# Kernel tuning notes

Hardware: AMD Instinct MI355X
Metric: run time of the kernel (lower is better)

The kernel has to match this reference:

```python
import jax, jax.numpy as jnp
import numpy as np

N_TOKENS = 2048
HIDDEN = 2880
N_HEADS = 64          # total query heads
N_KV = 8              # key/value heads
Q_MULT = N_HEADS // N_KV
HEAD_DIM = 64
SLIDING_WINDOW = 128  # layer_idx=0 -> sliding-window layer
SM_SCALE = 1.0 / np.sqrt(HEAD_DIM)
RMS_EPS = 1e-5
ROPE_BASE = 150000.0
ROPE_SCALING = 32.0
INIT_CTX = 4096
NTK_ALPHA = 1.0
NTK_BETA = 32.0


def _rope_tables(num_tokens):
    # YaRN NTK-by-parts inverse frequencies (static constants)
    freq = ROPE_BASE ** (np.arange(0, HEAD_DIM, 2, dtype=np.float64) / HEAD_DIM)
    concentration = 0.1 * np.log(ROPE_SCALING) + 1.0
    d_half = HEAD_DIM / 2
    low = d_half * np.log(INIT_CTX / (NTK_BETA * 2 * np.pi)) / np.log(ROPE_BASE)
    high = d_half * np.log(INIT_CTX / (NTK_ALPHA * 2 * np.pi)) / np.log(ROPE_BASE)
    interpolation = 1.0 / (ROPE_SCALING * freq)
    extrapolation = 1.0 / freq
    ramp = (np.arange(d_half) - low) / (high - low)
    m = 1.0 - np.clip(ramp, 0.0, 1.0)
    inv_freq = interpolation * (1.0 - m) + extrapolation * m
    t = np.arange(num_tokens, dtype=np.float64)
    freqs = np.outer(t, inv_freq)
    cos = jnp.asarray((np.cos(freqs) * concentration), dtype=jnp.float32)
    sin = jnp.asarray((np.sin(freqs) * concentration), dtype=jnp.float32)
    return cos, sin  # [num_tokens, HEAD_DIM//2]


def _apply_rotary(x, cos, sin):
    # x: [n, heads, HEAD_DIM]
    c = cos[:, None, :].astype(x.dtype)
    s = sin[:, None, :].astype(x.dtype)
    x1, x2 = jnp.split(x, 2, axis=-1)
    return jnp.concatenate([x1 * c - x2 * s, x2 * c + x1 * s], axis=-1)


def setup_inputs() -> dict:
    key = jax.random.key(0)
    ks = jax.random.split(key, 7)
    return {
        "x": jax.random.normal(ks[0], (N_TOKENS, HIDDEN), jnp.float32),
        "scale": jax.random.uniform(ks[1], (HIDDEN,), jnp.float32, 0.5, 1.5),
        "sink": jax.random.normal(ks[2], (N_HEADS,), jnp.float32),
        "w_qkv": jax.random.normal(ks[3], (HIDDEN, (N_HEADS + 2 * N_KV) * HEAD_DIM), jnp.float32) * 0.02,
        "b_qkv": jax.random.normal(ks[4], ((N_HEADS + 2 * N_KV) * HEAD_DIM,), jnp.float32) * 0.02,
        "w_o": jax.random.normal(ks[5], (N_HEADS * HEAD_DIM, HIDDEN), jnp.float32) * 0.02,
        "b_o": jax.random.normal(ks[6], (HIDDEN,), jnp.float32) * 0.02,
    }


def reference(x, scale, sink, w_qkv, b_qkv, w_o, b_o):
    n = x.shape[0]
    # RMSNorm (fp32)
    t = x.astype(jnp.float32)
    rms = jnp.sqrt(jnp.mean(t * t, axis=-1, keepdims=True) + RMS_EPS)
    t = (t / rms) * scale

    # QKV projection + split
    qkv = t @ w_qkv + b_qkv
    q_sz = N_HEADS * HEAD_DIM
    kv_sz = N_KV * HEAD_DIM
    q = qkv[:, :q_sz].reshape(n, N_HEADS, HEAD_DIM)
    k = qkv[:, q_sz:q_sz + kv_sz].reshape(n, N_KV, HEAD_DIM)
    v = qkv[:, q_sz + kv_sz:].reshape(n, N_KV, HEAD_DIM)

    # RoPE (YaRN)
    cos, sin = _rope_tables(n)
    q = _apply_rotary(q, cos, sin)
    k = _apply_rotary(k, cos, sin)

    # GQA layout: [n, N_KV, Q_MULT, HEAD_DIM]
    qg = q.reshape(n, N_KV, Q_MULT, HEAD_DIM)

    # scores: [N_KV, Q_MULT, n_q, n_kv]
    scores = jnp.einsum('nhgd,mhd->hgnm', qg, k) * SM_SCALE

    # causal + sliding-window mask
    q_pos = jnp.arange(n)[:, None]
    kv_pos = jnp.arange(n)[None, :]
    mask = jnp.where(kv_pos > q_pos, -jnp.inf, 0.0)
    mask = mask + jnp.where((SLIDING_WINDOW > 0) & (q_pos - kv_pos > SLIDING_WINDOW), -jnp.inf, 0.0)
    scores = scores + mask[None, None, :, :].astype(scores.dtype)

    # sink logit appended as extra softmax column, then dropped
    s_col = jnp.broadcast_to(sink.reshape(N_KV, Q_MULT, 1, 1), (N_KV, Q_MULT, n, 1))
    w = jax.nn.softmax(jnp.concatenate([scores, s_col], axis=-1), axis=-1)[..., :-1]

    attn = jnp.einsum('hgnm,mhd->nhgd', w, v).reshape(n, N_HEADS * HEAD_DIM)
    out = attn @ w_o + b_o
    return x + out


if __name__ == '__main__':
    inp = setup_inputs()
    y = reference(**inp)
    print(y.shape, y.dtype)
```

## Files before the change

### kernel.cpp

```cpp
#include <hip/hip_runtime.h>
#include <cstdint>
#include <cstddef>

#define HIDDEN   2880
#define QKV_N    5120
#define OPROJ_K  4096
#define NTOK     2048
#define WIN      128
#define SM_SCALE 0.125f

typedef _Float16 half8  __attribute__((ext_vector_type(8)));
typedef _Float16 half4v __attribute__((ext_vector_type(4)));
typedef float    f32x4  __attribute__((ext_vector_type(4)));

__device__ __forceinline__ void gload16(const void* g, void* l) {
  __builtin_amdgcn_global_load_lds((__attribute__((address_space(1))) void*)g,
                                   (__attribute__((address_space(3))) void*)l,
                                   16, 0, 0);
}

__device__ __forceinline__ _Float16 f2h(float f) { return (_Float16)f; }

#define NB_T0  (80 * 45)
#define NB_T1  (46 * 64)
#define NB_ROPE 256

__device__ __forceinline__ void cast_transpose64(const float* __restrict__ W,
                                                 _Float16* __restrict__ Wt,
                                                 int K, int N, int n0, int k0,
                                                 float* tile ) {
  int t = threadIdx.x;
  #pragma unroll
  for (int p = 0; p < 16; ++p) {
    int r = p * 4 + (t >> 6), cc = t & 63;
    float vv = 0.f;
    if (n0 + cc < N) vv = W[(size_t)(k0 + r) * N + n0 + cc];
    tile[r * 65 + cc] = vv;
  }
  __syncthreads();
  #pragma unroll
  for (int p = 0; p < 2; ++p) {
    int idx = p * 256 + t;
    int r = idx >> 3, ch = (idx & 7) * 8;
    half8 h;
    #pragma unroll
    for (int u = 0; u < 8; ++u) h[u] = (_Float16)tile[(ch + u) * 65 + r];
    *(half8*)&Wt[(size_t)(n0 + r) * K + k0 + ch] = h;
  }
}

__global__ __launch_bounds__(256) void prep_kernel(const float* __restrict__ x,
                                                   const float* __restrict__ scale,
                                                   const float* __restrict__ w_qkv,
                                                   const float* __restrict__ w_o,
                                                   _Float16* __restrict__ a_h,
                                                   _Float16* __restrict__ wtq,
                                                   _Float16* __restrict__ wto,
                                                   float2* __restrict__ tab) {
  __shared__ float smem[64 * 65];
  int b = blockIdx.x, t = threadIdx.x;
  if (b < NB_T0) {
    cast_transpose64(w_qkv, wtq, HIDDEN, QKV_N, (b % 80) * 64, (b / 80) * 64, smem);
    return;
  }
  b -= NB_T0;
  if (b < NB_T1) {
    cast_transpose64(w_o, wto, OPROJ_K, HIDDEN, (b % 46) * 64, (b / 46) * 64, smem);
    return;
  }
  b -= NB_T1;
  if (b < NTOK) {
    int row = b;
    const float4* xr = (const float4*)(x + (size_t)row * HIDDEN);
    const float4* sc = (const float4*)scale;
    float4 v0 = xr[t];
    float4 v1 = xr[t + 256];
    float4 v2 = (t < 208) ? xr[t + 512] : make_float4(0.f, 0.f, 0.f, 0.f);
    float ss = v0.x*v0.x + v0.y*v0.y + v0.z*v0.z + v0.w*v0.w
             + v1.x*v1.x + v1.y*v1.y + v1.z*v1.z + v1.w*v1.w
             + v2.x*v2.x + v2.y*v2.y + v2.z*v2.z + v2.w*v2.w;
    #pragma unroll
    for (int m = 1; m < 64; m <<= 1) ss += __shfl_xor(ss, m, 64);
    if ((t & 63) == 0) smem[t >> 6] = ss;
    __syncthreads();
    float inv = 1.0f / sqrtf((smem[0] + smem[1] + smem[2] + smem[3]) * (1.0f / HIDDEN) + 1e-5f);
    _Float16* orow = a_h + (size_t)row * HIDDEN;
    auto store4 = [&](int c4, const float4& v, const float4& s) {
      half4v h;
      h[0] = f2h(v.x * inv * s.x); h[1] = f2h(v.y * inv * s.y);
      h[2] = f2h(v.z * inv * s.z); h[3] = f2h(v.w * inv * s.w);
      *(half4v*)(orow + (size_t)c4 * 4) = h;
    };
    store4(t, v0, sc[t]);
    store4(t + 256, v1, sc[t + 256]);
    if (t < 208) store4(t + 512, v2, sc[t + 512]);
    return;
  }
  b -= NTOK;
  {
    int idx = b * 256 + t;
    int tok = idx >> 5, d = idx & 31;
    const double PI = 3.14159265358979323846;
    double i = (double)d;
    double lf = log(150000.0);
    double freq = exp(lf * (i / 32.0));
    double interp = 1.0 / (32.0 * freq);
    double extrap = 1.0 / freq;
    double low  = 32.0 * log(4096.0 / (32.0 * 2.0 * PI)) / lf;
    double high = 32.0 * log(4096.0 / (2.0 * PI)) / lf;
    double ramp = (i - low) / (high - low);
    double mm = 1.0 - fmin(fmax(ramp, 0.0), 1.0);
    double invf = interp * (1.0 - mm) + extrap * mm;
    double ang = (double)tok * invf;
    double conc = 0.1 * log(32.0) + 1.0;
    tab[idx] = make_float2((float)(cos(ang) * conc), (float)(sin(ang) * conc));
  }
}

template <int BM, bool QKV_MODE, int MINW, bool SWZ>
__global__ __launch_bounds__(256, MINW) void gemm_kernel(const _Float16* __restrict__ A,
                                                         const _Float16* __restrict__ Bt,
                                                         const float* __restrict__ bias,
                                                         const float* __restrict__ resid,
                                                         const float2* __restrict__ tab,
                                                         void* __restrict__ Cout,
                                                         int M, int N, int K) {
  constexpr int MI = BM / 32;
  constexpr int NA = BM / 32;
  __shared__ _Float16 Alds[BM * 64];
  __shared__ _Float16 Blds[128 * 64];
  int tid = threadIdx.x;
  int wave = tid >> 6, lane = tid & 63;
  int wm = wave >> 1, wn = wave & 1;
  int c = lane & 15, quad = lane >> 4;
  int bx = blockIdx.x, by = blockIdx.y;
  if (SWZ) {
    int gx = gridDim.x;
    int flat = by * gx + bx;
    int n8 = (gx * gridDim.y) >> 3;
    int swz = (flat & 7) * n8 + (flat >> 3);
    bx = swz % gx; by = swz / gx;
  }
  int m0 = by * BM, n0 = bx * 128;

  const _Float16* gAp[NA]; _Float16* lAp[NA];
  #pragma unroll
  for (int i = 0; i < NA; ++i) {
    int p = wave * 64 + i * 256 + lane;
    int r = p >> 3;
    int kl = (p & 7) ^ (r & 7);
    gAp[i] = A + (size_t)(m0 + r) * K + kl * 8;
    lAp[i] = Alds + (size_t)(wave * 64 + i * 256) * 8;
  }
  const _Float16* gBp[4]; _Float16* lBp[4];
  #pragma unroll
  for (int i = 0; i < 4; ++i) {
    int p = wave * 64 + i * 256 + lane;
    int r = p >> 3;
    int kl = (p & 7) ^ (r & 7);
    gBp[i] = Bt + (size_t)(n0 + r) * K + kl * 8;
    lBp[i] = Blds + (size_t)(wave * 64 + i * 256) * 8;
  }

  int px[2];
  px[0] = ((0 * 4 + quad) ^ (c & 7)) * 8;
  px[1] = ((1 * 4 + quad) ^ (c & 7)) * 8;

  f32x4 acc[MI][4] = {};
  int nIter = K >> 6;
  for (int kt = 0; kt < nIter; ++kt) {
    __syncthreads();
    #pragma unroll
    for (int i = 0; i < NA; ++i) { gload16(gAp[i], lAp[i]); gAp[i] += 64; }
    #pragma unroll
    for (int i = 0; i < 4; ++i)  { gload16(gBp[i], lBp[i]); gBp[i] += 64; }
    __syncthreads();
    half8 a[MI][2], b[4][2];
    #pragma unroll
    for (int i = 0; i < MI; ++i) {
      int row = wm * (BM / 2) + i * 16 + c;
      a[i][0] = *(const half8*)&Alds[row * 64 + px[0]];
      a[i][1] = *(const half8*)&Alds[row * 64 + px[1]];
    }
    #pragma unroll
    for (int j = 0; j < 4; ++j) {
      int row = wn * 64 + j * 16 + c;
      b[j][0] = *(const half8*)&Blds[row * 64 + px[0]];
      b[j][1] = *(const half8*)&Blds[row * 64 + px[1]];
    }
    #pragma unroll
    for (int i = 0; i < MI; ++i)
      #pragma unroll
      for (int j = 0; j < 4; ++j) {
        acc[i][j] = __builtin_amdgcn_mfma_f32_16x16x32_f16(a[i][0], b[j][0], acc[i][j], 0, 0, 0);
        acc[i][j] = __builtin_amdgcn_mfma_f32_16x16x32_f16(a[i][1], b[j][1], acc[i][j], 0, 0, 0);
      }
  }

  if (QKV_MODE) {
    _Float16* outp = (_Float16*)Cout;
    bool ropeTile = (n0 < 4608);
    #pragma unroll
    for (int i = 0; i < MI; ++i) {
      int rowb = m0 + wm * (BM / 2) + i * 16 + quad * 4;
      if (ropeTile) {
        #pragma unroll
        for (int jp = 0; jp < 2; ++jp) {
          int col = n0 + wn * 64 + jp * 16 + c;
          float b1 = bias[col], b2 = bias[col + 32];
          #pragma unroll
          for (int r = 0; r < 4; ++r) {
            float2 cs = tab[(size_t)(rowb + r) * 32 + jp * 16 + c];
            float x1 = acc[i][jp][r] + b1;
            float x2 = acc[i][jp + 2][r] + b2;
            outp[(size_t)(rowb + r) * QKV_N + col]      = f2h(x1 * cs.x - x2 * cs.y);
            outp[(size_t)(rowb + r) * QKV_N + col + 32] = f2h(x2 * cs.x + x1 * cs.y);
          }
        }
      } else {
        #pragma unroll
        for (int j = 0; j < 4; ++j) {
          int col = n0 + wn * 64 + j * 16 + c;
          float bv = bias[col];
          #pragma unroll
          for (int r = 0; r < 4; ++r)
            outp[(size_t)(rowb + r) * QKV_N + col] = f2h(acc[i][j][r] + bv);
        }
      }
    }
  } else {
    float* outp = (float*)Cout;
    #pragma unroll
    for (int i = 0; i < MI; ++i) {
      int rowb = m0 + wm * (BM / 2) + i * 16 + quad * 4;
      #pragma unroll
      for (int j = 0; j < 4; ++j) {
        int col = n0 + wn * 64 + j * 16 + c;
        if (col < N) {
          float bv = bias[col];
          #pragma unroll
          for (int r = 0; r < 4; ++r)
            outp[(size_t)(rowb + r) * N + col] =
                acc[i][j][r] + bv + resid[(size_t)(rowb + r) * N + col];
        }
      }
    }
  }
}

#define TQ 16
__global__ __launch_bounds__(256) void attn_kernel(const _Float16* __restrict__ qkv,
                                                   const float* __restrict__ sink,
                                                   _Float16* __restrict__ attn_out) {
  __shared__ __align__(16) char smem[61440];
  _Float16* Klds = (_Float16*)smem;
  _Float16* Qlds = (_Float16*)(smem + 20480);
  _Float16* Ps   = (_Float16*)smem;
  _Float16* Vt   = (_Float16*)(smem + 40960);

  int qt = blockIdx.x, kvh = blockIdx.y;
  int Q0 = qt * TQ;
  int kmin = (Q0 >= WIN) ? Q0 - WIN : 0;
  int nkv = Q0 + TQ - kmin;
  int tid = threadIdx.x;
  int wave = tid >> 6, lane = tid & 63;
  int c = lane & 15, quad = lane >> 4;

  {
    const _Float16* kbase = qkv + 4096 + kvh * 64;
    #pragma unroll
    for (int p = 0; p < 5; ++p) {
      int ci = p * 256 + wave * 64 + lane;
      int row = ci >> 3, pc = ci & 7;
      int lc = pc ^ (row & 7);
      gload16(kbase + (size_t)(kmin + row) * QKV_N + lc * 8,
              (char*)Klds + (size_t)(p * 256 + wave * 64) * 16);
    }
  }
  {
    const _Float16* qbase = qkv + kvh * 512;
    #pragma unroll
    for (int p = 0; p < 4; ++p) {
      int ci = p * 256 + wave * 64 + lane;
      int tok = ci >> 6, Lp = ci & 63;
      int Llog = (Lp & 56) | ((Lp ^ tok) & 7);
      gload16(qbase + (size_t)(Q0 + tok) * QKV_N + Llog * 8,
              (char*)Qlds + (size_t)(p * 256 + wave * 64) * 16);
    }
  }
  #pragma unroll
  for (int p = 0; p < 5; ++p) {
    int cc = p * 256 + tid;
    int col = cc % 160;
    int d0 = (cc / 160) * 8;
    union { uint4 u4; _Float16 hv[8]; } buf;
    if (col < nkv) buf.u4 = *(const uint4*)(qkv + (size_t)(kmin + col) * QKV_N + 4608 + kvh * 64 + d0);
    else           buf.u4 = make_uint4(0, 0, 0, 0);
    #pragma unroll
    for (int uu = 0; uu < 8; ++uu) Vt[(d0 + uu) * 160 + col] = buf.hv[uu];
  }

  __syncthreads();

  half8 aq[2][2];
  #pragma unroll
  for (int i = 0; i < 2; ++i) {
    int qm = wave * 2 + i;
    #pragma unroll
    for (int ks = 0; ks < 2; ++ks) {
      int kc = ks * 4 + quad;
      int Lp = qm * 8 + (kc ^ (c & 7));
      aq[i][ks] = *(const half8*)&Qlds[c * 512 + Lp * 8];
    }
  }

  f32x4 sacc[2][9] = {};
  #pragma unroll
  for (int j = 0; j < 9; ++j) {
    #pragma unroll
    for (int ks = 0; ks < 2; ++ks) {
      int kc = ks * 4 + quad;
      int pc = kc ^ (c & 7);
      half8 bk = *(const half8*)&Klds[(j * 16 + c) * 64 + pc * 8];
      #pragma unroll
      for (int i = 0; i < 2; ++i)
        sacc[i][j] = __builtin_amdgcn_mfma_f32_16x16x32_f16(aq[i][ks], bk, sacc[i][j], 0, 0, 0);
    }
  }

  __syncthreads();

  #pragma unroll
  for (int p = 0; p < 8; ++p) {
    int idx = p * 256 + tid;
    Ps[(idx >> 4) * 160 + 144 + (idx & 15)] = (_Float16)0.f;
  }

  #pragma unroll
  for (int i = 0; i < 2; ++i) {
    int qm = wave * 2 + i;
    float sk = sink[kvh * 8 + qm];
    #pragma unroll
    for (int r = 0; r < 4; ++r) {
      int qpos = Q0 + quad * 4 + r;
      float sv[9]; float mx = -3e38f;
      #pragma unroll
      for (int j = 0; j < 9; ++j) {
        int key = kmin + j * 16 + c;
        float s = sacc[i][j][r] * SM_SCALE;
        bool valid = (key <= qpos) && (qpos - key <= WIN);
        sv[j] = valid ? s : -3e38f;
        mx = fmaxf(mx, sv[j]);
      }
      #pragma unroll
      for (int msk = 1; msk < 16; msk <<= 1) mx = fmaxf(mx, __shfl_xor(mx, msk, 64));
      mx = fmaxf(mx, sk);
      float sum = 0.f; float pv[9];
      #pragma unroll
      for (int j = 0; j < 9; ++j) { float p = __expf(sv[j] - mx); pv[j] = p; sum += p; }
      #pragma unroll
      for (int msk = 1; msk < 16; msk <<= 1) sum += __shfl_xor(sum, msk, 64);
      sum += __expf(sk - mx);
      float inv = 1.0f / sum;
      int mrow = qm * 16 + quad * 4 + r;
      #pragma unroll
      for (int j = 0; j < 9; ++j)
        Ps[mrow * 160 + j * 16 + c] = f2h(pv[j] * inv);
    }
  }

  __syncthreads();

  f32x4 oacc[2][4] = {};
  #pragma unroll
  for (int ks = 0; ks < 5; ++ks) {
    half8 ap[2], bv[4];
    #pragma unroll
    for (int i = 0; i < 2; ++i)
      ap[i] = *(const half8*)&Ps[((wave * 2 + i) * 16 + c) * 160 + ks * 32 + quad * 8];
    #pragma unroll
    for (int j = 0; j < 4; ++j)
      bv[j] = *(const half8*)&Vt[(j * 16 + c) * 160 + ks * 32 + quad * 8];
    #pragma unroll
    for (int i = 0; i < 2; ++i)
      #pragma unroll
      for (int j = 0; j < 4; ++j)
        oacc[i][j] = __builtin_amdgcn_mfma_f32_16x16x32_f16(ap[i], bv[j], oacc[i][j], 0, 0, 0);
  }

  #pragma unroll
  for (int i = 0; i < 2; ++i) {
    int qm = wave * 2 + i;
    #pragma unroll
    for (int j = 0; j < 4; ++j)
      #pragma unroll
      for (int r = 0; r < 4; ++r) {
        int token = Q0 + quad * 4 + r;
        attn_out[(size_t)token * 4096 + (kvh * 8 + qm) * 64 + j * 16 + c] = f2h(oacc[i][j][r]);
      }
  }
}

extern "C" void kernel_launch(void* const* d_in, const int* in_sizes, int n_in,
                              void* d_out, int out_size, void* d_ws, size_t ws_size,
                              hipStream_t stream) {
  (void)in_sizes; (void)n_in; (void)out_size; (void)ws_size;
  const float* x      = (const float*)d_in[0];
  const float* scale  = (const float*)d_in[1];
  const float* sink   = (const float*)d_in[2];
  const float* w_qkv  = (const float*)d_in[3];
  const float* b_qkv  = (const float*)d_in[4];
  const float* w_o    = (const float*)d_in[5];
  const float* b_o    = (const float*)d_in[6];
  float* out = (float*)d_out;

  char* ws = (char*)d_ws;
  size_t off = 0;
  auto alloc = [&](size_t bytes) { void* p = ws + off; off += (bytes + 255) & ~(size_t)255; return p; };
  _Float16* wtq   = (_Float16*)alloc((size_t)QKV_N * HIDDEN * 2);
  _Float16* wto   = (_Float16*)alloc((size_t)2944 * OPROJ_K * 2);
  _Float16* a_h   = (_Float16*)alloc((size_t)NTOK * HIDDEN * 2);
  _Float16* qkv_h = (_Float16*)alloc((size_t)NTOK * QKV_N * 2);
  float2*   tab   = (float2*)alloc((size_t)NTOK * 32 * sizeof(float2));
  _Float16* at_h  = (_Float16*)wtq;

  int prep_blocks = NB_T0 + NB_T1 + NTOK + NB_ROPE;
  prep_kernel<<<prep_blocks, 256, 0, stream>>>(x, scale, w_qkv, w_o, a_h, wtq, wto, tab);
  gemm_kernel<128, true, 3, false><<<dim3(QKV_N / 128, NTOK / 128), 256, 0, stream>>>(
      a_h, wtq, b_qkv, nullptr, tab, qkv_h, NTOK, QKV_N, HIDDEN);
  attn_kernel<<<dim3(NTOK / TQ, 8), 256, 0, stream>>>(qkv_h, sink, at_h);
  gemm_kernel<128, false, 3, true><<<dim3(23, NTOK / 128), 256, 0, stream>>>(
      at_h, wto, b_o, x, nullptr, out, NTOK, HIDDEN, OPROJ_K);
}
```

Baseline: 345.6 us.

## Use 8 waves per attention block and smaller M tile for output projection

The attention kernel now runs 512 threads so each wave owns one query head instead of two, which halves per-wave register use and doubles parallelism inside a block. The grid is flattened to 1D with kv-head as the fast index so neighbouring blocks share a query tile. The LDS row stride for P and transposed V is padded from 160 to 164 to reduce bank conflicts. The output projection GEMM switches to a 64-row tile with a different pipeline-depth parameter, giving more blocks for the 2048x2880 output at the cost of less reuse per block.

```diff
diff --git a/kernel.cpp b/kernel.cpp
--- a/kernel.cpp
+++ b/kernel.cpp
@@ -249,72 +249,75 @@
 }
 
 #define TQ 16
-__global__ __launch_bounds__(256) void attn_kernel(const _Float16* __restrict__ qkv,
+#define PSTR 164
+__global__ __launch_bounds__(512) void attn_kernel(const _Float16* __restrict__ qkv,
                                                    const float* __restrict__ sink,
                                                    _Float16* __restrict__ attn_out) {
-  __shared__ __align__(16) char smem[61440];
+  __shared__ __align__(16) char smem[62976];
   _Float16* Klds = (_Float16*)smem;
   _Float16* Qlds = (_Float16*)(smem + 20480);
   _Float16* Ps   = (_Float16*)smem;
-  _Float16* Vt   = (_Float16*)(smem + 40960);
-
-  int qt = blockIdx.x, kvh = blockIdx.y;
+  _Float16* Vt   = (_Float16*)(smem + 41984);
+
+  int aidx = blockIdx.x;
+  int qt = aidx >> 3, kvh = aidx & 7;
   int Q0 = qt * TQ;
   int kmin = (Q0 >= WIN) ? Q0 - WIN : 0;
   int nkv = Q0 + TQ - kmin;
   int tid = threadIdx.x;
   int wave = tid >> 6, lane = tid & 63;
   int c = lane & 15, quad = lane >> 4;
+  int qm = wave;
 
   {
     const _Float16* kbase = qkv + 4096 + kvh * 64;
     #pragma unroll
-    for (int p = 0; p < 5; ++p) {
-      int ci = p * 256 + wave * 64 + lane;
-      int row = ci >> 3, pc = ci & 7;
-      int lc = pc ^ (row & 7);
-      gload16(kbase + (size_t)(kmin + row) * QKV_N + lc * 8,
-              (char*)Klds + (size_t)(p * 256 + wave * 64) * 16);
+    for (int p = 0; p < 3; ++p) {
+      int ci = p * 512 + tid;
+      if (ci < 1280) {
+        int row = ci >> 3, pc = ci & 7;
+        int lc = pc ^ (row & 7);
+        gload16(kbase + (size_t)(kmin + row) * QKV_N + lc * 8,
+                (char*)Klds + (size_t)(p * 512 + wave * 64) * 16);
+      }
     }
   }
   {
     const _Float16* qbase = qkv + kvh * 512;
     #pragma unroll
-    for (int p = 0; p < 4; ++p) {
-      int ci = p * 256 + wave * 64 + lane;
+    for (int p = 0; p < 2; ++p) {
+      int ci = p * 512 + tid;
       int tok = ci >> 6, Lp = ci & 63;
       int Llog = (Lp & 56) | ((Lp ^ tok) & 7);
       gload16(qbase + (size_t)(Q0 + tok) * QKV_N + Llog * 8,
-              (char*)Qlds + (size_t)(p * 256 + wave * 64) * 16);
-    }
-  }
-  #pragma unroll
-  for (int p = 0; p < 5; ++p) {
-    int cc = p * 256 + tid;
-    int col = cc % 160;
-    int d0 = (cc / 160) * 8;
-    union { uint4 u4; _Float16 hv[8]; } buf;
-    if (col < nkv) buf.u4 = *(const uint4*)(qkv + (size_t)(kmin + col) * QKV_N + 4608 + kvh * 64 + d0);
-    else           buf.u4 = make_uint4(0, 0, 0, 0);
-    #pragma unroll
-    for (int uu = 0; uu < 8; ++uu) Vt[(d0 + uu) * 160 + col] = buf.hv[uu];
+              (char*)Qlds + (size_t)(p * 512 + wave * 64) * 16);
+    }
+  }
+  #pragma unroll
+  for (int p = 0; p < 3; ++p) {
+    int cc = p * 512 + tid;
+    if (cc < 1280) {
+      int col = cc % 160;
+      int d0 = (cc / 160) * 8;
+      union { uint4 u4; _Float16 hv[8]; } buf;
+      if (col < nkv) buf.u4 = *(const uint4*)(qkv + (size_t)(kmin + col) * QKV_N + 4608 + kvh * 64 + d0);
+      else           buf.u4 = make_uint4(0, 0, 0, 0);
+      #pragma unroll
+      for (int uu = 0; uu < 8; ++uu) Vt[(d0 + uu) * PSTR + col] = buf.hv[uu];
+    }
   }
 
   __syncthreads();
 
-  half8 aq[2][2];
-  #pragma unroll
-  for (int i = 0; i < 2; ++i) {
-    int qm = wave * 2 + i;
-    #pragma unroll
-    for (int ks = 0; ks < 2; ++ks) {
-      int kc = ks * 4 + quad;
-      int Lp = qm * 8 + (kc ^ (c & 7));
-      aq[i][ks] = *(const half8*)&Qlds[c * 512 + Lp * 8];
-    }
-  }
-
-  f32x4 sacc[2][9] = {};
+  half8 aq[2];
+  #pragma unroll
+  for (int ks = 0; ks < 2; ++ks) {
+    int kc = ks * 4 + quad;
+    int Lp = qm * 8 + (kc ^ (c & 7));
+    aq[ks] = *(const half8*)&Qlds[c * 512 + Lp * 8];
+  }
+
+  f32x4 sacc[9] = {};
   #pragma unroll
   for (int j = 0; j < 9; ++j) {
     #pragma unroll
@@ -322,23 +325,19 @@
       int kc = ks * 4 + quad;
       int pc = kc ^ (c & 7);
       half8 bk = *(const half8*)&Klds[(j * 16 + c) * 64 + pc * 8];
-      #pragma unroll
-      for (int i = 0; i < 2; ++i)
-        sacc[i][j] = __builtin_amdgcn_mfma_f32_16x16x32_f16(aq[i][ks], bk, sacc[i][j], 0, 0, 0);
+      sacc[j] = __builtin_amdgcn_mfma_f32_16x16x32_f16(aq[ks], bk, sacc[j], 0, 0, 0);
     }
   }
 
   __syncthreads();
 
   #pragma unroll
-  for (int p = 0; p < 8; ++p) {
-    int idx = p * 256 + tid;
-    Ps[(idx >> 4) * 160 + 144 + (idx & 15)] = (_Float16)0.f;
-  }
-
-  #pragma unroll
-  for (int i = 0; i < 2; ++i) {
-    int qm = wave * 2 + i;
+  for (int p = 0; p < 4; ++p) {
+    int idx = p * 512 + tid;
+    Ps[(idx >> 4) * PSTR + 144 + (idx & 15)] = (_Float16)0.f;
+  }
+
+  {
     float sk = sink[kvh * 8 + qm];
     #pragma unroll
     for (int r = 0; r < 4; ++r) {
@@ -347,7 +346,7 @@
       #pragma unroll
       for (int j = 0; j < 9; ++j) {
         int key = kmin + j * 16 + c;
-        float s = sacc[i][j][r] * SM_SCALE;
+        float s = sacc[j][r] * SM_SCALE;
         bool valid = (key <= qpos) && (qpos - key <= WIN);
         sv[j] = valid ? s : -3e38f;
         mx = fmaxf(mx, sv[j]);
@@ -365,40 +364,32 @@
       int mrow = qm * 16 + quad * 4 + r;
       #pragma unroll
       for (int j = 0; j < 9; ++j)
-        Ps[mrow * 160 + j * 16 + c] = f2h(pv[j] * inv);
+        Ps[mrow * PSTR + j * 16 + c] = f2h(pv[j] * inv);
     }
   }
 
   __syncthreads();
 
-  f32x4 oacc[2][4] = {};
+  f32x4 oacc[4] = {};
   #pragma unroll
   for (int ks = 0; ks < 5; ++ks) {
-    half8 ap[2], bv[4];
-    #pragma unroll
-    for (int i = 0; i < 2; ++i)
-      ap[i] = *(const half8*)&Ps[((wave * 2 + i) * 16 + c) * 160 + ks * 32 + quad * 8];
+    half8 ap = *(const half8*)&Ps[(qm * 16 + c) * PSTR + ks * 32 + quad * 8];
+    half8 bv[4];
     #pragma unroll
     for (int j = 0; j < 4; ++j)
-      bv[j] = *(const half8*)&Vt[(j * 16 + c) * 160 + ks * 32 + quad * 8];
-    #pragma unroll
-    for (int i = 0; i < 2; ++i)
-      #pragma unroll
-      for (int j = 0; j < 4; ++j)
-        oacc[i][j] = __builtin_amdgcn_mfma_f32_16x16x32_f16(ap[i], bv[j], oacc[i][j], 0, 0, 0);
-  }
-
-  #pragma unroll
-  for (int i = 0; i < 2; ++i) {
-    int qm = wave * 2 + i;
+      bv[j] = *(const half8*)&Vt[(j * 16 + c) * PSTR + ks * 32 + quad * 8];
     #pragma unroll
     for (int j = 0; j < 4; ++j)
-      #pragma unroll
-      for (int r = 0; r < 4; ++r) {
-        int token = Q0 + quad * 4 + r;
-        attn_out[(size_t)token * 4096 + (kvh * 8 + qm) * 64 + j * 16 + c] = f2h(oacc[i][j][r]);
-      }
-  }
+      oacc[j] = __builtin_amdgcn_mfma_f32_16x16x32_f16(ap, bv[j], oacc[j], 0, 0, 0);
+  }
+
+  #pragma unroll
+  for (int j = 0; j < 4; ++j)
+    #pragma unroll
+    for (int r = 0; r < 4; ++r) {
+      int token = Q0 + quad * 4 + r;
+      attn_out[(size_t)token * 4096 + (kvh * 8 + qm) * 64 + j * 16 + c] = f2h(oacc[j][r]);
+    }
 }
 
 extern "C" void kernel_launch(void* const* d_in, const int* in_sizes, int n_in,
@@ -428,7 +419,7 @@
   prep_kernel<<<prep_blocks, 256, 0, stream>>>(x, scale, w_qkv, w_o, a_h, wtq, wto, tab);
   gemm_kernel<128, true, 3, false><<<dim3(QKV_N / 128, NTOK / 128), 256, 0, stream>>>(
       a_h, wtq, b_qkv, nullptr, tab, qkv_h, NTOK, QKV_N, HIDDEN);
-  attn_kernel<<<dim3(NTOK / TQ, 8), 256, 0, stream>>>(qkv_h, sink, at_h);
-  gemm_kernel<128, false, 3, true><<<dim3(23, NTOK / 128), 256, 0, stream>>>(
+  attn_kernel<<<dim3((NTOK / TQ) * 8), 512, 0, stream>>>(qkv_h, sink, at_h);
+  gemm_kernel<64, false, 4, true><<<dim3(23, NTOK / 64), 256, 0, stream>>>(
       at_h, wto, b_o, x, nullptr, out, NTOK, HIDDEN, OPROJ_K);
 }
```

Measured after the change: 345.1 us. No clear change (-0.2%).
